# Performance work log

Measured on AMD Instinct MI355X. Metric: run time of the kernel, lower is better.

Reference implementation:

```python
import jax, jax.numpy as jnp
import numpy as np

SIGMA = 2.0
INF = 1.0e6
M, N, H, K, C_IN, C_OUT = 50000, 100000, 32, 15, 64, 64
RADIUS = 2.5


def setup_inputs() -> dict:
    key = jax.random.key(0)
    k1, k2, k3, k4, k5, k6 = jax.random.split(key, 6)
    q_points = jax.random.normal(k1, (M, 3), dtype=jnp.float32)
    s_points = jax.random.normal(k2, (N, 3), dtype=jnp.float32)
    s_feats = jax.random.normal(k3, (N, C_IN), dtype=jnp.float32)
    # index N refers to the padding point (placed at INF)
    neighbor_indices = jax.random.randint(k4, (M, H), 0, N + 1, dtype=jnp.int64)
    weights = jax.random.normal(k5, (K, C_IN, C_OUT), dtype=jnp.float32) * 0.05
    # kernel points inside sphere of RADIUS (stand-in for load_kernels buffer)
    kp = jax.random.normal(k6, (K, 3), dtype=jnp.float32)
    kp = kp / jnp.linalg.norm(kp, axis=1, keepdims=True) * RADIUS * 0.7
    kernel_points = kp.at[0].set(0.0)  # fixed='center'
    return {
        "q_points": q_points,
        "s_points": s_points,
        "s_feats": s_feats,
        "neighbor_indices": neighbor_indices,
        "weights": weights,
        "kernel_points": kernel_points,
    }


def reference(q_points, s_points, s_feats, neighbor_indices, weights, kernel_points):
    # pad support points with an 'infinity' shadow point at index N
    padded_pts = jnp.concatenate([s_points, jnp.full((1, 3), INF, s_points.dtype)], axis=0)
    neighbors = padded_pts[neighbor_indices]                    # (M, H, 3)
    rel = neighbors - q_points[:, None, :]                      # (M, H, 3)
    diff = rel[:, :, None, :] - kernel_points[None, None]       # (M, H, K, 3)
    sq_dist = jnp.sum(diff * diff, axis=-1)                     # (M, H, K)
    nbr_w = jnp.clip(1.0 - jnp.sqrt(sq_dist) / SIGMA, 0.0)      # (M, H, K)

    padded_feats = jnp.concatenate([s_feats, jnp.zeros((1, s_feats.shape[1]), s_feats.dtype)], axis=0)
    nbr_feats = padded_feats[neighbor_indices]                  # (M, H, C_in)

    weighted = jnp.einsum('mhk,mhc->mkc', nbr_w, nbr_feats)     # (M, K, C_in)
    out = jnp.einsum('mkc,kcd->md', weighted, weights)          # (M, C_out)

    # normalize by count of real (non-padding / nonzero-sum) neighbors
    nbr_sum = jnp.sum(nbr_feats, axis=-1)                       # (M, H)
    nbr_num = jnp.sum(nbr_sum > 0.0, axis=-1)                   # (M,)
    nbr_num = jnp.maximum(nbr_num, 1)
    return out / nbr_num[:, None].astype(out.dtype)
```

## Files before the change

kernel.cpp:

```cpp
#include <hip/hip_runtime.h>
#include <hip/hip_bf16.h>

#define MPTS 50000
#define NPTS 100000
#define KK 15
#define TM 8
#define WTP 1036
#define STP 36

typedef __attribute__((ext_vector_type(8))) short short8;
typedef __attribute__((ext_vector_type(4))) short short4v;
typedef __attribute__((ext_vector_type(4))) float floatx4;

static __device__ __forceinline__ unsigned short f2bf(float f) {
    __hip_bfloat16 h = __float2bfloat16(f);
    return *reinterpret_cast<unsigned short*>(&h);
}

static __device__ __forceinline__ short8 lds_load8(const unsigned short* p) {
    const short4v a = *(const short4v*)p;
    const short4v b = *(const short4v*)(p + 4);
    short8 r;
    r[0] = a[0]; r[1] = a[1]; r[2] = a[2]; r[3] = a[3];
    r[4] = b[0]; r[5] = b[1]; r[6] = b[2]; r[7] = b[3];
    return r;
}

__global__ void prep_all(const float* __restrict__ sf, const float* __restrict__ w,
                         const float* __restrict__ kpts,
                         unsigned short* __restrict__ sfb, float* __restrict__ rs,
                         unsigned short* __restrict__ wbf2, float4* __restrict__ kpp) {
    const int b = blockIdx.x, t = threadIdx.x;
    if (b < 782) {
        const int tt = b * 256 + t;
        const int row = tt >> 1, p = tt & 1;
        if (row < NPTS) {
            const float* base = sf + (size_t)row * 64 + p * 4;
            float4 r = *(const float4*)base;
            {
                ushort4 o;
                o.x = f2bf(r.x); o.y = f2bf(r.y); o.z = f2bf(r.z); o.w = f2bf(r.w);
                *(ushort4*)&sfb[(size_t)row * 64 + p * 4] = o;
            }
#pragma unroll
            for (int i = 1; i < 8; i++) {
                const float4 x = *(const float4*)(base + i * 8);
                ushort4 o;
                o.x = f2bf(x.x); o.y = f2bf(x.y); o.z = f2bf(x.z); o.w = f2bf(x.w);
                *(ushort4*)&sfb[(size_t)row * 64 + i * 8 + p * 4] = o;
                r.x += x.x; r.y += x.y; r.z += x.z; r.w += x.w;
            }
            float sp = (r.x + r.y) + (r.z + r.w);
            sp += __shfl_xor(sp, 1);
            if (p == 0) rs[row] = sp;
        }
    } else if (b < 814) {
        const int e = (b - 782) * 256 + t;
        const int lane = e & 63, s = (e >> 6) & 31, wq = e >> 11;
        const int d = wq * 16 + (lane & 15);
        const int lqp = lane >> 4;
        unsigned short o8[8];
#pragma unroll
        for (int j = 0; j < 8; j++) {
            const int kc = s * 32 + lqp * 8 + j;
            const int c = kc >> 4, k = kc & 15;
            o8[j] = (k < KK) ? f2bf(w[k * 4096 + c * 64 + d]) : (unsigned short)0;
        }
#pragma unroll
        for (int j = 0; j < 8; j++) wbf2[(size_t)e * 8 + j] = o8[j];
    } else {
        if (t < 16) *(ushort4*)&sfb[(size_t)NPTS * 64 + t * 4] = make_ushort4(0, 0, 0, 0);
        else if (t == 16) rs[NPTS] = -1.0f;
        else if (t >= 32 && t < 32 + KK) {
            const int k = t - 32;
            const float kx = kpts[k * 3 + 0], ky = kpts[k * 3 + 1], kz = kpts[k * 3 + 2];
            kpp[k] = make_float4(-2.f * kx, -2.f * ky, -2.f * kz, kx * kx + ky * ky + kz * kz);
        }
    }
}

__global__ __launch_bounds__(256, 4) void kpconv_fused(
    const float* __restrict__ q_points,
    const float* __restrict__ s_points,
    const unsigned short* __restrict__ sfb,
    const int*   __restrict__ nbr,
    const unsigned short* __restrict__ wbf2,
    const float4* __restrict__ kpp,
    const float* __restrict__ rowsum,
    float* __restrict__ out)
{
    const int t    = threadIdx.x;
    const int m0   = blockIdx.x * TM;
    const int lane = t & 63;
    const int wv   = t >> 6;
    const int l15  = lane & 15;
    const int lq   = lane >> 4;

    __shared__ int idx_lds[TM][32];
    __shared__ unsigned short stage[4][64 * STP];
    __shared__ unsigned short wtw[TM * WTP];
    __shared__ float inv_lds[TM];

    const int mw = 2 * wv + (lane >> 5);
    const int h  = lane & 31;
    idx_lds[mw][h] = nbr[(size_t)(m0 + mw) * 32 + h];

    ushort4 g[2][8];
    const int c4 = l15 * 4;
#pragma unroll
    for (int mi = 0; mi < 2; mi++) {
        const int m = 2 * wv + mi;
#pragma unroll
        for (int g2 = 0; g2 < 4; g2++) {
            const int r0 = g2 * 8 + lq * 2;
            const int2 ip = *(const int2*)&idx_lds[m][r0];
            const int i0 = min(ip.x, NPTS);
            const int i1 = min(ip.y, NPTS);
            g[mi][2 * g2]     = *(const ushort4*)&sfb[(size_t)i0 * 64 + c4];
            g[mi][2 * g2 + 1] = *(const ushort4*)&sfb[(size_t)i1 * 64 + c4];
        }
    }

    {
        const int idx = idx_lds[mw][h];
        float px = 1.0e6f, py = 1.0e6f, pz = 1.0e6f;
        if (idx < NPTS) {
            px = s_points[idx * 3 + 0];
            py = s_points[idx * 3 + 1];
            pz = s_points[idx * 3 + 2];
        }
        const float rx = px - q_points[(m0 + mw) * 3 + 0];
        const float ry = py - q_points[(m0 + mw) * 3 + 1];
        const float rz = pz - q_points[(m0 + mw) * 3 + 2];
        const float r2 = rx * rx + ry * ry + rz * rz;
        unsigned short* wrow = &wtw[mw * WTP];
#pragma unroll
        for (int k = 0; k < KK; k++) {
            const float4 kp = kpp[k];
            float d2 = kp.w;
            d2 = fmaf(rx, kp.x, d2);
            d2 = fmaf(ry, kp.y, d2);
            d2 = fmaf(rz, kp.z, d2);
            d2 = fmaxf(r2 + d2, 0.0f);
            const float wv_ = fmaxf(fmaf(-0.5f, __builtin_amdgcn_sqrtf(d2), 1.0f), 0.0f);
            wrow[k * STP + h] = f2bf(wv_);
        }
        wrow[15 * STP + h] = 0;

        const bool ok = rowsum[min(idx, NPTS)] > 0.0f;
        const unsigned long long bal = __ballot(ok);
        if (h == 0) {
            const int cnt = __popc((unsigned)(bal >> ((lane >> 5) * 32)));
            inv_lds[mw] = 1.0f / (float)(cnt < 1 ? 1 : cnt);
        }
    }

    unsigned short* const st = stage[wv];
    const int swzw = (l15 >> 2) << 2;
#pragma unroll
    for (int mi = 0; mi < 2; mi++) {
        const int m = 2 * wv + mi;

#pragma unroll
        for (int g2 = 0; g2 < 4; g2++) {
            const int so = ((g2 * 4 + lq) ^ swzw) * 2;
            const ushort4 a = g[mi][2 * g2];
            const ushort4 b = g[mi][2 * g2 + 1];
            *(unsigned*)&st[(c4 + 0) * STP + so] = (unsigned)a.x | ((unsigned)b.x << 16);
            *(unsigned*)&st[(c4 + 1) * STP + so] = (unsigned)a.y | ((unsigned)b.y << 16);
            *(unsigned*)&st[(c4 + 2) * STP + so] = (unsigned)a.z | ((unsigned)b.z << 16);
            *(unsigned*)&st[(c4 + 3) * STP + so] = (unsigned)a.w | ((unsigned)b.w << 16);
        }

        const short8 afrag = lds_load8(&wtw[m * WTP + l15 * STP + lq * 8]);
#pragma unroll
        for (int ct = 0; ct < 4; ct++) {
            const short8 bfrag = lds_load8(&st[(ct * 16 + l15) * STP + ((lq ^ ct) * 8)]);
            floatx4 d = {0.f, 0.f, 0.f, 0.f};
            d = __builtin_amdgcn_mfma_f32_16x16x32_bf16(afrag, bfrag, d, 0, 0, 0);
            ushort4 pk;
            pk.x = f2bf(d[0]); pk.y = f2bf(d[1]); pk.z = f2bf(d[2]); pk.w = f2bf(d[3]);
            *(ushort4*)&wtw[m * WTP + (ct * 16 + l15) * 16 + lq * 4] = pk;
        }
    }
    __syncthreads();

    {
        floatx4 acc = {0.f, 0.f, 0.f, 0.f};
        const unsigned short* ap = &wtw[(l15 & 7) * WTP + lq * 8];
        const unsigned short* bp = wbf2 + ((size_t)(wv * 32) * 64 + lane) * 8;
#pragma unroll 8
        for (int s = 0; s < 32; s++) {
            const short8 a = lds_load8(ap + s * 32);
            const short8 b = *(const short8*)(bp + s * 512);
            acc = __builtin_amdgcn_mfma_f32_16x16x32_bf16(a, b, acc, 0, 0, 0);
        }
        if (lq < 2) {
            const int d = wv * 16 + l15;
#pragma unroll
            for (int r = 0; r < 4; r++) {
                const int m = lq * 4 + r;
                out[(size_t)(m0 + m) * 64 + d] = acc[r] * inv_lds[m];
            }
        }
    }
}

extern "C" void kernel_launch(void* const* d_in, const int* in_sizes, int n_in,
                              void* d_out, int out_size, void* d_ws, size_t ws_size,
                              hipStream_t stream) {
    const float* q_points = (const float*)d_in[0];
    const float* s_points = (const float*)d_in[1];
    const float* s_feats  = (const float*)d_in[2];
    const int*   nbr      = (const int*)d_in[3];
    const float* weights  = (const float*)d_in[4];
    const float* kpts     = (const float*)d_in[5];
    float* out = (float*)d_out;

    char* ws = (char*)d_ws;
    unsigned short* wbf2 = (unsigned short*)ws;
    float* rowsum = (float*)(ws + 131072);
    float4* kpp = (float4*)(ws + 531600);
    unsigned short* sfb = (unsigned short*)(ws + 532480);

    prep_all<<<815, 256, 0, stream>>>(s_feats, weights, kpts, sfb, rowsum, wbf2, kpp);
    kpconv_fused<<<MPTS / TM, 256, 0, stream>>>(q_points, s_points, sfb, nbr,
                                                wbf2, kpp, rowsum, out);
}
```

Baseline: 148.2 us.

## Fill the 16-row MFMA tile with 16 points per block and split the weight GEMM over K

The block now handles 16 query points with 512 threads instead of 8 points with 256. The final weight GEMM previously used only 8 of the 16 MFMA rows. Now all 16 rows carry real points, so each bf16 weight fragment fetched from global memory serves twice as many points. That GEMM's reduction dimension is split between two groups of four waves, and the partial sums are combined through LDS scratch with an extra barrier. The support-point coordinate loads are also moved ahead of the feature gathers to start that latency earlier. The cost is a larger LDS footprint per block and more register pressure under the new launch bounds, which could lower occupancy.

```diff
diff --git a/kernel.cpp b/kernel.cpp
--- a/kernel.cpp
+++ b/kernel.cpp
@@ -4,7 +4,7 @@
 #define MPTS 50000
 #define NPTS 100000
 #define KK 15
-#define TM 8
+#define TM 16
 #define WTP 1036
 #define STP 36
 
@@ -79,7 +79,7 @@
     }
 }
 
-__global__ __launch_bounds__(256, 4) void kpconv_fused(
+__global__ __launch_bounds__(512, 4) void kpconv_fused(
     const float* __restrict__ q_points,
     const float* __restrict__ s_points,
     const unsigned short* __restrict__ sfb,
@@ -97,13 +97,21 @@
     const int lq   = lane >> 4;
 
     __shared__ int idx_lds[TM][32];
-    __shared__ unsigned short stage[4][64 * STP];
+    __shared__ __align__(16) unsigned short stage[8][64 * STP];
     __shared__ unsigned short wtw[TM * WTP];
     __shared__ float inv_lds[TM];
 
     const int mw = 2 * wv + (lane >> 5);
     const int h  = lane & 31;
     idx_lds[mw][h] = nbr[(size_t)(m0 + mw) * 32 + h];
+
+    const int idxp = idx_lds[mw][h];
+    float px = 1.0e6f, py = 1.0e6f, pz = 1.0e6f;
+    if (idxp < NPTS) {
+        px = s_points[idxp * 3 + 0];
+        py = s_points[idxp * 3 + 1];
+        pz = s_points[idxp * 3 + 2];
+    }
 
     ushort4 g[2][8];
     const int c4 = l15 * 4;
@@ -122,13 +130,6 @@
     }
 
     {
-        const int idx = idx_lds[mw][h];
-        float px = 1.0e6f, py = 1.0e6f, pz = 1.0e6f;
-        if (idx < NPTS) {
-            px = s_points[idx * 3 + 0];
-            py = s_points[idx * 3 + 1];
-            pz = s_points[idx * 3 + 2];
-        }
         const float rx = px - q_points[(m0 + mw) * 3 + 0];
         const float ry = py - q_points[(m0 + mw) * 3 + 1];
         const float rz = pz - q_points[(m0 + mw) * 3 + 2];
@@ -147,7 +148,7 @@
         }
         wrow[15 * STP + h] = 0;
 
-        const bool ok = rowsum[min(idx, NPTS)] > 0.0f;
+        const bool ok = rowsum[min(idxp, NPTS)] > 0.0f;
         const unsigned long long bal = __ballot(ok);
         if (h == 0) {
             const int cnt = __popc((unsigned)(bal >> ((lane >> 5) * 32)));
@@ -186,21 +187,30 @@
     __syncthreads();
 
     {
+        const int q  = wv & 3;
+        const int kh = wv >> 2;
         floatx4 acc = {0.f, 0.f, 0.f, 0.f};
-        const unsigned short* ap = &wtw[(l15 & 7) * WTP + lq * 8];
-        const unsigned short* bp = wbf2 + ((size_t)(wv * 32) * 64 + lane) * 8;
+        const unsigned short* ap = &wtw[l15 * WTP + kh * 512 + lq * 8];
+        const unsigned short* bp = wbf2 + ((size_t)((q * 32 + kh * 16) * 64) + lane) * 8;
 #pragma unroll 8
-        for (int s = 0; s < 32; s++) {
+        for (int s = 0; s < 16; s++) {
             const short8 a = lds_load8(ap + s * 32);
             const short8 b = *(const short8*)(bp + s * 512);
             acc = __builtin_amdgcn_mfma_f32_16x16x32_bf16(a, b, acc, 0, 0, 0);
         }
-        if (lq < 2) {
-            const int d = wv * 16 + l15;
+
+        float* const scratch = (float*)&stage[0][0];
+        if (kh == 1) {
+            *(floatx4*)&scratch[q * 256 + l15 * 16 + lq * 4] = acc;
+        }
+        __syncthreads();
+        if (kh == 0) {
+            const floatx4 p = *(const floatx4*)&scratch[q * 256 + l15 * 16 + lq * 4];
+            const int d = q * 16 + l15;
 #pragma unroll
             for (int r = 0; r < 4; r++) {
                 const int m = lq * 4 + r;
-                out[(size_t)(m0 + m) * 64 + d] = acc[r] * inv_lds[m];
+                out[(size_t)(m0 + m) * 64 + d] = (acc[r] + p[r]) * inv_lds[m];
             }
         }
     }
@@ -224,6 +234,6 @@
     unsigned short* sfb = (unsigned short*)(ws + 532480);
 
     prep_all<<<815, 256, 0, stream>>>(s_feats, weights, kpts, sfb, rowsum, wbf2, kpp);
-    kpconv_fused<<<MPTS / TM, 256, 0, stream>>>(q_points, s_points, sfb, nbr,
+    kpconv_fused<<<MPTS / TM, 512, 0, stream>>>(q_points, s_points, sfb, nbr,
                                                 wbf2, kpp, rowsum, out);
 }
```

Result: faster. 142.2 us (-4.1%).
